# Kernel tuning notes

Hardware: AMD Instinct MI355X
Metric: run time of the kernel (lower is better)

The kernel has to match this reference:

```python
import jax, jax.numpy as jnp
import numpy as np


def setup_inputs() -> dict:
    key = jax.random.key(0)
    k1, k2, k3 = jax.random.split(key, 3)
    T, B, E = 2048, 2, 1024
    x = jax.random.normal(k1, (T, B, E), dtype=jnp.float32)
    # xavier-uniform-ish scaled weights
    in_weight = jax.random.normal(k2, (3 * E, E), dtype=jnp.float32) * (1.0 / np.sqrt(E))
    in_bias = jnp.zeros((3 * E,), dtype=jnp.float32)
    out_weight = jax.random.normal(k3, (E, E), dtype=jnp.float32) * (1.0 / np.sqrt(E))
    out_bias = jnp.zeros((E,), dtype=jnp.float32)
    return {"x": x, "in_weight": in_weight, "in_bias": in_bias,
            "out_weight": out_weight, "out_bias": out_bias, "n_heads": 16}


def reference(x, in_weight, in_bias, out_weight, out_bias, n_heads):
    # x: [T, B, E] time-major, self-attention (query is key is value)
    T, B, E = x.shape
    H = n_heads
    hd = E // H
    scale = hd ** -0.5
    # fused in-projection: [T, B, 3E]
    qkv = jnp.einsum('tbe,fe->tbf', x, in_weight) + in_bias
    q, k, v = jnp.split(qkv, 3, axis=-1)
    q = q * scale
    # [T, B, E] -> [B*H, T, hd]
    def to_heads(t):
        return t.reshape(T, B * H, hd).transpose(1, 0, 2)
    q, k, v = to_heads(q), to_heads(k), to_heads(v)
    # attention scores [B*H, T, T]
    attn_weights = jnp.einsum('nqd,nkd->nqk', q, k)
    attn_weights = jax.nn.softmax(attn_weights, axis=-1)
    # dropout p=0.0 (eval) -> identity
    attn = jnp.einsum('nqk,nkd->nqd', attn_weights, v)  # [B*H, T, hd]
    attn = attn.transpose(1, 0, 2).reshape(T, B, E)
    out = jnp.einsum('tbe,fe->tbf', attn, out_weight) + out_bias
    # need_weights=True: average over heads -> [B, T, T]
    avg_weights = attn_weights.reshape(B, H, T, T).sum(axis=1) / H
    return out, avg_weights
```

## Files before the change

kernel.cpp:

```cpp
#include <hip/hip_runtime.h>


#define T_DIM 2048
#define B_DIM 2
#define E_DIM 1024
#define H_DIM 16
#define HD 64
#define F_DIM 3072
#define M_DIM (T_DIM * B_DIM)
#define SCALE 0.125f

typedef __attribute__((ext_vector_type(8))) short bf16x8;
typedef __attribute__((ext_vector_type(4))) float f32x4;

__device__ inline unsigned short f2bf(float f) {
    union { float f; unsigned u; } v; v.f = f;
    unsigned r = v.u + 0x7fff + ((v.u >> 16) & 1);
    return (unsigned short)(r >> 16);
}

__global__ __launch_bounds__(256) void cast_bf16(
    const float* __restrict__ src, unsigned short* __restrict__ dst, int n8)
{
    int i = blockIdx.x * 256 + threadIdx.x;
    if (i >= n8) return;
    float4 a = *(const float4*)&src[i * 8];
    float4 b = *(const float4*)&src[i * 8 + 4];
    bf16x8 o;
    o[0] = f2bf(a.x); o[1] = f2bf(a.y); o[2] = f2bf(a.z); o[3] = f2bf(a.w);
    o[4] = f2bf(b.x); o[5] = f2bf(b.y); o[6] = f2bf(b.z); o[7] = f2bf(b.w);
    *(bf16x8*)&dst[i * 8] = o;
}

template <int MODE>
__global__ __launch_bounds__(256) void gemm_bf16(
    const unsigned short* __restrict__ A, const unsigned short* __restrict__ W,
    const float* __restrict__ bias,
    unsigned short* __restrict__ qb, unsigned short* __restrict__ kb,
    unsigned short* __restrict__ vb, float* __restrict__ outp)
{
    __shared__ short As[128][72];
    __shared__ short Bs[128][72];

    const int tid  = threadIdx.x;
    const int lane = tid & 63;
    const int wv   = tid >> 6;
    const int l16  = lane & 15;
    const int g    = lane >> 4;
    const int wr   = wv >> 1, wc = wv & 1;
    const int n0   = blockIdx.x * 128, m0 = blockIdx.y * 128;

    const int srow = tid >> 2;
    const int sc   = (tid & 3) * 16;

    f32x4 acc[4][4] = {};

    for (int k0 = 0; k0 < E_DIM; k0 += 64) {
        __syncthreads();
#pragma unroll
        for (int i = 0; i < 2; ++i) {
            const int row = srow + i * 64;
            const size_t ga = (size_t)(m0 + row) * E_DIM + k0 + sc;
            const size_t gb = (size_t)(n0 + row) * E_DIM + k0 + sc;
            *(bf16x8*)&As[row][sc]     = *(const bf16x8*)&A[ga];
            *(bf16x8*)&As[row][sc + 8] = *(const bf16x8*)&A[ga + 8];
            *(bf16x8*)&Bs[row][sc]     = *(const bf16x8*)&W[gb];
            *(bf16x8*)&Bs[row][sc + 8] = *(const bf16x8*)&W[gb + 8];
        }
        __syncthreads();

        bf16x8 af[4][2], bf[4][2];
#pragma unroll
        for (int mt = 0; mt < 4; ++mt) {
            af[mt][0] = *(const bf16x8*)&As[wr * 64 + mt * 16 + l16][g * 8];
            af[mt][1] = *(const bf16x8*)&As[wr * 64 + mt * 16 + l16][32 + g * 8];
        }
#pragma unroll
        for (int nt = 0; nt < 4; ++nt) {
            bf[nt][0] = *(const bf16x8*)&Bs[wc * 64 + nt * 16 + l16][g * 8];
            bf[nt][1] = *(const bf16x8*)&Bs[wc * 64 + nt * 16 + l16][32 + g * 8];
        }
#pragma unroll
        for (int mt = 0; mt < 4; ++mt)
#pragma unroll
            for (int nt = 0; nt < 4; ++nt) {
                acc[mt][nt] = __builtin_amdgcn_mfma_f32_16x16x32_bf16(
                    af[mt][0], bf[nt][0], acc[mt][nt], 0, 0, 0);
                acc[mt][nt] = __builtin_amdgcn_mfma_f32_16x16x32_bf16(
                    af[mt][1], bf[nt][1], acc[mt][nt], 0, 0, 0);
            }
    }

#pragma unroll
    for (int mt = 0; mt < 4; ++mt)
#pragma unroll
        for (int nt = 0; nt < 4; ++nt)
#pragma unroll
            for (int rr = 0; rr < 4; ++rr) {
                const int r = m0 + wr * 64 + mt * 16 + g * 4 + rr;
                const int f = n0 + wc * 64 + nt * 16 + l16;
                float val = acc[mt][nt][rr] + bias[f];
                if (MODE == 0) {
                    const int t = r >> 1, b = r & 1;
                    const int sec = f >> 10, rem = f & 1023;
                    const int h = rem >> 6, d = rem & 63;
                    const size_t idx = ((size_t)(b * H_DIM + h) * T_DIM + t) * HD + d;
                    if (sec == 0)      qb[idx] = f2bf(val * SCALE);
                    else if (sec == 1) kb[idx] = f2bf(val);
                    else               vb[idx] = f2bf(val);
                } else {
                    outp[(size_t)r * E_DIM + f] = val;
                }
            }
}

__global__ __launch_bounds__(256) void flash_kernel(
    const unsigned short* __restrict__ qb, const unsigned short* __restrict__ kb,
    const unsigned short* __restrict__ vb, unsigned short* __restrict__ ctxbuf,
    float2* __restrict__ ml)
{
    __shared__ short Ks[64][72];
    __shared__ short Vt[64][72];
    __shared__ short Ps[64][72];

    const int tid  = threadIdx.x;
    const int lane = tid & 63;
    const int w    = tid >> 6;
    const int l16  = lane & 15;
    const int g    = lane >> 4;
    const int q0   = blockIdx.x * 64;
    const int n    = blockIdx.y;
    const int b    = n >> 4, h = n & 15;

    const int krow = tid >> 2, kd0 = (tid & 3) << 4;
    const int vrow = tid & 63, vd0 = (tid >> 6) << 4;

    const size_t qrow = (size_t)n * T_DIM + q0 + w * 16 + l16;
    bf16x8 qf0 = *(const bf16x8*)&qb[qrow * HD + g * 8];
    bf16x8 qf1 = *(const bf16x8*)&qb[qrow * HD + 32 + g * 8];

    f32x4 ctx[4] = {};
    float m_[4], l_[4];
#pragma unroll
    for (int r = 0; r < 4; ++r) { m_[r] = -1e30f; l_[r] = 0.f; }

    for (int kt = 0; kt < T_DIM; kt += 64) {
        __syncthreads();
        const size_t kgrow = (size_t)n * T_DIM + kt;
        *(bf16x8*)&Ks[krow][kd0]     = *(const bf16x8*)&kb[(kgrow + krow) * HD + kd0];
        *(bf16x8*)&Ks[krow][kd0 + 8] = *(const bf16x8*)&kb[(kgrow + krow) * HD + kd0 + 8];
        bf16x8 v0 = *(const bf16x8*)&vb[(kgrow + vrow) * HD + vd0];
        bf16x8 v1 = *(const bf16x8*)&vb[(kgrow + vrow) * HD + vd0 + 8];
#pragma unroll
        for (int e = 0; e < 8; ++e) {
            Vt[vd0 + e][vrow]     = v0[e];
            Vt[vd0 + 8 + e][vrow] = v1[e];
        }
        __syncthreads();

        f32x4 s[4];
#pragma unroll
        for (int nt = 0; nt < 4; ++nt) {
            bf16x8 kf0 = *(const bf16x8*)&Ks[nt * 16 + l16][g * 8];
            bf16x8 kf1 = *(const bf16x8*)&Ks[nt * 16 + l16][32 + g * 8];
            f32x4 z = {0.f, 0.f, 0.f, 0.f};
            z = __builtin_amdgcn_mfma_f32_16x16x32_bf16(qf0, kf0, z, 0, 0, 0);
            z = __builtin_amdgcn_mfma_f32_16x16x32_bf16(qf1, kf1, z, 0, 0, 0);
            s[nt] = z;
        }

        float p[4][4];
#pragma unroll
        for (int r = 0; r < 4; ++r) {
            float mt = fmaxf(fmaxf(s[0][r], s[1][r]), fmaxf(s[2][r], s[3][r]));
            mt = fmaxf(mt, __shfl_xor(mt, 1));
            mt = fmaxf(mt, __shfl_xor(mt, 2));
            mt = fmaxf(mt, __shfl_xor(mt, 4));
            mt = fmaxf(mt, __shfl_xor(mt, 8));
            float mnew = fmaxf(m_[r], mt);
            float f = __expf(m_[r] - mnew);
            float rs = 0.f;
#pragma unroll
            for (int nt = 0; nt < 4; ++nt) { p[nt][r] = __expf(s[nt][r] - mnew); rs += p[nt][r]; }
            rs += __shfl_xor(rs, 1);
            rs += __shfl_xor(rs, 2);
            rs += __shfl_xor(rs, 4);
            rs += __shfl_xor(rs, 8);
            l_[r] = l_[r] * f + rs;
            m_[r] = mnew;
#pragma unroll
            for (int dt = 0; dt < 4; ++dt) ctx[dt][r] *= f;
        }

#pragma unroll
        for (int nt = 0; nt < 4; ++nt)
#pragma unroll
            for (int r = 0; r < 4; ++r)
                Ps[w * 16 + g * 4 + r][nt * 16 + l16] = (short)f2bf(p[nt][r]);

        bf16x8 pa0 = *(const bf16x8*)&Ps[w * 16 + l16][g * 8];
        bf16x8 pa1 = *(const bf16x8*)&Ps[w * 16 + l16][32 + g * 8];
#pragma unroll
        for (int dt = 0; dt < 4; ++dt) {
            bf16x8 vf0 = *(const bf16x8*)&Vt[dt * 16 + l16][g * 8];
            bf16x8 vf1 = *(const bf16x8*)&Vt[dt * 16 + l16][32 + g * 8];
            ctx[dt] = __builtin_amdgcn_mfma_f32_16x16x32_bf16(pa0, vf0, ctx[dt], 0, 0, 0);
            ctx[dt] = __builtin_amdgcn_mfma_f32_16x16x32_bf16(pa1, vf1, ctx[dt], 0, 0, 0);
        }
    }

    float linv[4];
#pragma unroll
    for (int r = 0; r < 4; ++r) linv[r] = 1.0f / l_[r];

#pragma unroll
    for (int dt = 0; dt < 4; ++dt)
#pragma unroll
        for (int r = 0; r < 4; ++r) {
            const int q = q0 + w * 16 + g * 4 + r;
            const int d = dt * 16 + l16;
            ctxbuf[((size_t)q * B_DIM + b) * E_DIM + h * HD + d] = f2bf(ctx[dt][r] * linv[r]);
        }

    if (l16 == 0) {
#pragma unroll
        for (int r = 0; r < 4; ++r)
            ml[(size_t)n * T_DIM + q0 + w * 16 + g * 4 + r] = make_float2(m_[r], linv[r]);
    }
}

__global__ __launch_bounds__(256) void avg_kernel(
    const unsigned short* __restrict__ qb, const unsigned short* __restrict__ kb,
    const float2* __restrict__ ml, float* __restrict__ avg)
{
    __shared__ short Kh[64][72];

    const int tid  = threadIdx.x;
    const int lane = tid & 63;
    const int w    = tid >> 6;
    const int l16  = lane & 15;
    const int g    = lane >> 4;
    const int kt0  = blockIdx.x * 64;
    const int q0   = blockIdx.y * 64;
    const int b    = blockIdx.z;

    const int krow = tid >> 2, kd0 = (tid & 3) << 4;

    f32x4 acc[4] = {};

    for (int h = 0; h < H_DIM; ++h) {
        const int n = b * H_DIM + h;
        __syncthreads();
        const size_t kgrow = (size_t)n * T_DIM + kt0;
        *(bf16x8*)&Kh[krow][kd0]     = *(const bf16x8*)&kb[(kgrow + krow) * HD + kd0];
        *(bf16x8*)&Kh[krow][kd0 + 8] = *(const bf16x8*)&kb[(kgrow + krow) * HD + kd0 + 8];
        __syncthreads();

        const size_t qrow = (size_t)n * T_DIM + q0 + w * 16 + l16;
        bf16x8 qf0 = *(const bf16x8*)&qb[qrow * HD + g * 8];
        bf16x8 qf1 = *(const bf16x8*)&qb[qrow * HD + 32 + g * 8];

        float2 mlv[4];
#pragma unroll
        for (int r = 0; r < 4; ++r)
            mlv[r] = ml[(size_t)n * T_DIM + q0 + w * 16 + g * 4 + r];

#pragma unroll
        for (int nt = 0; nt < 4; ++nt) {
            bf16x8 kf0 = *(const bf16x8*)&Kh[nt * 16 + l16][g * 8];
            bf16x8 kf1 = *(const bf16x8*)&Kh[nt * 16 + l16][32 + g * 8];
            f32x4 z = {0.f, 0.f, 0.f, 0.f};
            z = __builtin_amdgcn_mfma_f32_16x16x32_bf16(qf0, kf0, z, 0, 0, 0);
            z = __builtin_amdgcn_mfma_f32_16x16x32_bf16(qf1, kf1, z, 0, 0, 0);
#pragma unroll
            for (int r = 0; r < 4; ++r)
                acc[nt][r] += __expf(z[r] - mlv[r].x) * mlv[r].y * (1.0f / H_DIM);
        }
    }

#pragma unroll
    for (int nt = 0; nt < 4; ++nt)
#pragma unroll
        for (int r = 0; r < 4; ++r) {
            const int q = q0 + w * 16 + g * 4 + r;
            avg[((size_t)b * T_DIM + q) * T_DIM + kt0 + nt * 16 + l16] = acc[nt][r];
        }
}

extern "C" void kernel_launch(void* const* d_in, const int* in_sizes, int n_in,
                              void* d_out, int out_size, void* d_ws, size_t ws_size,
                              hipStream_t stream)
{
    const float* x     = (const float*)d_in[0];
    const float* w_in  = (const float*)d_in[1];
    const float* b_in  = (const float*)d_in[2];
    const float* w_out = (const float*)d_in[3];
    const float* b_out = (const float*)d_in[4];

    float* out = (float*)d_out;
    float* avg = out + (size_t)T_DIM * B_DIM * E_DIM;

    const size_t HSZ = (size_t)B_DIM * H_DIM * T_DIM * HD;
    unsigned short* qb   = (unsigned short*)d_ws;
    unsigned short* kb   = qb + HSZ;
    unsigned short* vb   = kb + HSZ;
    unsigned short* ctxb = vb + HSZ;
    unsigned short* xb   = ctxb + (size_t)T_DIM * B_DIM * E_DIM;
    unsigned short* wbin = xb + (size_t)T_DIM * B_DIM * E_DIM;
    unsigned short* wbot = wbin + (size_t)F_DIM * E_DIM;
    float2* ml = (float2*)(wbot + (size_t)E_DIM * E_DIM);

    cast_bf16<<<(T_DIM * B_DIM * E_DIM / 8 + 255) / 256, 256, 0, stream>>>(
        x, xb, T_DIM * B_DIM * E_DIM / 8);
    cast_bf16<<<(F_DIM * E_DIM / 8 + 255) / 256, 256, 0, stream>>>(
        w_in, wbin, F_DIM * E_DIM / 8);
    cast_bf16<<<(E_DIM * E_DIM / 8 + 255) / 256, 256, 0, stream>>>(
        w_out, wbot, E_DIM * E_DIM / 8);

    gemm_bf16<0><<<dim3(F_DIM / 128, M_DIM / 128), 256, 0, stream>>>(
        xb, wbin, b_in, qb, kb, vb, nullptr);

    flash_kernel<<<dim3(T_DIM / 64, B_DIM * H_DIM), 256, 0, stream>>>(
        qb, kb, vb, ctxb, ml);

    avg_kernel<<<dim3(T_DIM / 64, T_DIM / 64, B_DIM), 256, 0, stream>>>(
        qb, kb, ml, avg);

    gemm_bf16<1><<<dim3(E_DIM / 128, M_DIM / 128), 256, 0, stream>>>(
        ctxb, wbot, b_out, nullptr, nullptr, nullptr, out);
}
```

Measured before the change: 328.5 us.

## Prefetch K/V tiles into registers and widen avg kernel query tile

The flash kernel now loads the next K/V tile into registers while the current tile is written to shared memory and computed on, hiding global load latency. The avg kernel likewise prefetches the next head's K tile and processes 128 query rows per block instead of 64, halving the grid and reusing each staged K tile across two query sub-tiles. The bf16 conversion helper now calls the library __float2bfloat16 routine. The changes raise register pressure, which may reduce occupancy.

Result: slower. 338.0 us (+2.9%).

```diff
diff --git a/kernel.cpp b/kernel.cpp
--- a/kernel.cpp
+++ b/kernel.cpp
@@ -1,4 +1,5 @@
 #include <hip/hip_runtime.h>
+#include <hip/hip_bf16.h>
 
 
 #define T_DIM 2048
@@ -14,9 +15,9 @@
 typedef __attribute__((ext_vector_type(4))) float f32x4;
 
 __device__ inline unsigned short f2bf(float f) {
-    union { float f; unsigned u; } v; v.f = f;
-    unsigned r = v.u + 0x7fff + ((v.u >> 16) & 1);
-    return (unsigned short)(r >> 16);
+    union { __hip_bfloat16 h; unsigned short u; } v;
+    v.h = __float2bfloat16(f);
+    return v.u;
 }
 
 __global__ __launch_bounds__(256) void cast_bf16(
@@ -144,17 +145,27 @@
 #pragma unroll
     for (int r = 0; r < 4; ++r) { m_[r] = -1e30f; l_[r] = 0.f; }
 
+    const size_t hbase = (size_t)n * T_DIM;
+    bf16x8 kreg0 = *(const bf16x8*)&kb[(hbase + krow) * HD + kd0];
+    bf16x8 kreg1 = *(const bf16x8*)&kb[(hbase + krow) * HD + kd0 + 8];
+    bf16x8 vreg0 = *(const bf16x8*)&vb[(hbase + vrow) * HD + vd0];
+    bf16x8 vreg1 = *(const bf16x8*)&vb[(hbase + vrow) * HD + vd0 + 8];
+
     for (int kt = 0; kt < T_DIM; kt += 64) {
         __syncthreads();
-        const size_t kgrow = (size_t)n * T_DIM + kt;
-        *(bf16x8*)&Ks[krow][kd0]     = *(const bf16x8*)&kb[(kgrow + krow) * HD + kd0];
-        *(bf16x8*)&Ks[krow][kd0 + 8] = *(const bf16x8*)&kb[(kgrow + krow) * HD + kd0 + 8];
-        bf16x8 v0 = *(const bf16x8*)&vb[(kgrow + vrow) * HD + vd0];
-        bf16x8 v1 = *(const bf16x8*)&vb[(kgrow + vrow) * HD + vd0 + 8];
+        *(bf16x8*)&Ks[krow][kd0]     = kreg0;
+        *(bf16x8*)&Ks[krow][kd0 + 8] = kreg1;
 #pragma unroll
         for (int e = 0; e < 8; ++e) {
-            Vt[vd0 + e][vrow]     = v0[e];
-            Vt[vd0 + 8 + e][vrow] = v1[e];
+            Vt[vd0 + e][vrow]     = vreg0[e];
+            Vt[vd0 + 8 + e][vrow] = vreg1[e];
+        }
+        if (kt + 64 < T_DIM) {
+            const size_t kg = hbase + kt + 64;
+            kreg0 = *(const bf16x8*)&kb[(kg + krow) * HD + kd0];
+            kreg1 = *(const bf16x8*)&kb[(kg + krow) * HD + kd0 + 8];
+            vreg0 = *(const bf16x8*)&vb[(kg + vrow) * HD + vd0];
+            vreg1 = *(const bf16x8*)&vb[(kg + vrow) * HD + vd0 + 8];
         }
         __syncthreads();
 
@@ -241,50 +252,62 @@
     const int l16  = lane & 15;
     const int g    = lane >> 4;
     const int kt0  = blockIdx.x * 64;
-    const int q0   = blockIdx.y * 64;
+    const int q0   = blockIdx.y * 128;
     const int b    = blockIdx.z;
 
     const int krow = tid >> 2, kd0 = (tid & 3) << 4;
 
-    f32x4 acc[4] = {};
+    f32x4 acc[2][4] = {};
+
+    bf16x8 kreg0 = *(const bf16x8*)&kb[((size_t)(b * H_DIM) * T_DIM + kt0 + krow) * HD + kd0];
+    bf16x8 kreg1 = *(const bf16x8*)&kb[((size_t)(b * H_DIM) * T_DIM + kt0 + krow) * HD + kd0 + 8];
 
     for (int h = 0; h < H_DIM; ++h) {
         const int n = b * H_DIM + h;
         __syncthreads();
-        const size_t kgrow = (size_t)n * T_DIM + kt0;
-        *(bf16x8*)&Kh[krow][kd0]     = *(const bf16x8*)&kb[(kgrow + krow) * HD + kd0];
-        *(bf16x8*)&Kh[krow][kd0 + 8] = *(const bf16x8*)&kb[(kgrow + krow) * HD + kd0 + 8];
-        __syncthreads();
-
-        const size_t qrow = (size_t)n * T_DIM + q0 + w * 16 + l16;
-        bf16x8 qf0 = *(const bf16x8*)&qb[qrow * HD + g * 8];
-        bf16x8 qf1 = *(const bf16x8*)&qb[qrow * HD + 32 + g * 8];
-
-        float2 mlv[4];
-#pragma unroll
-        for (int r = 0; r < 4; ++r)
-            mlv[r] = ml[(size_t)n * T_DIM + q0 + w * 16 + g * 4 + r];
-
-#pragma unroll
-        for (int nt = 0; nt < 4; ++nt) {
-            bf16x8 kf0 = *(const bf16x8*)&Kh[nt * 16 + l16][g * 8];
-            bf16x8 kf1 = *(const bf16x8*)&Kh[nt * 16 + l16][32 + g * 8];
-            f32x4 z = {0.f, 0.f, 0.f, 0.f};
-            z = __builtin_amdgcn_mfma_f32_16x16x32_bf16(qf0, kf0, z, 0, 0, 0);
-            z = __builtin_amdgcn_mfma_f32_16x16x32_bf16(qf1, kf1, z, 0, 0, 0);
+        *(bf16x8*)&Kh[krow][kd0]     = kreg0;
+        *(bf16x8*)&Kh[krow][kd0 + 8] = kreg1;
+        if (h + 1 < H_DIM) {
+            const size_t kg = (size_t)(n + 1) * T_DIM + kt0 + krow;
+            kreg0 = *(const bf16x8*)&kb[kg * HD + kd0];
+            kreg1 = *(const bf16x8*)&kb[kg * HD + kd0 + 8];
+        }
+        __syncthreads();
+
+#pragma unroll
+        for (int qt = 0; qt < 2; ++qt) {
+            const size_t qrow = (size_t)n * T_DIM + q0 + qt * 64 + w * 16 + l16;
+            bf16x8 qf0 = *(const bf16x8*)&qb[qrow * HD + g * 8];
+            bf16x8 qf1 = *(const bf16x8*)&qb[qrow * HD + 32 + g * 8];
+
+            float2 mlv[4];
 #pragma unroll
             for (int r = 0; r < 4; ++r)
-                acc[nt][r] += __expf(z[r] - mlv[r].x) * mlv[r].y * (1.0f / H_DIM);
+                mlv[r] = ml[(size_t)n * T_DIM + q0 + qt * 64 + w * 16 + g * 4 + r];
+
+#pragma unroll
+            for (int nt = 0; nt < 4; ++nt) {
+                bf16x8 kf0 = *(const bf16x8*)&Kh[nt * 16 + l16][g * 8];
+                bf16x8 kf1 = *(const bf16x8*)&Kh[nt * 16 + l16][32 + g * 8];
+                f32x4 z = {0.f, 0.f, 0.f, 0.f};
+                z = __builtin_amdgcn_mfma_f32_16x16x32_bf16(qf0, kf0, z, 0, 0, 0);
+                z = __builtin_amdgcn_mfma_f32_16x16x32_bf16(qf1, kf1, z, 0, 0, 0);
+#pragma unroll
+                for (int r = 0; r < 4; ++r)
+                    acc[qt][nt][r] += __expf(z[r] - mlv[r].x) * mlv[r].y * (1.0f / H_DIM);
+            }
         }
     }
 
 #pragma unroll
-    for (int nt = 0; nt < 4; ++nt)
-#pragma unroll
-        for (int r = 0; r < 4; ++r) {
-            const int q = q0 + w * 16 + g * 4 + r;
-            avg[((size_t)b * T_DIM + q) * T_DIM + kt0 + nt * 16 + l16] = acc[nt][r];
-        }
+    for (int qt = 0; qt < 2; ++qt)
+#pragma unroll
+        for (int nt = 0; nt < 4; ++nt)
+#pragma unroll
+            for (int r = 0; r < 4; ++r) {
+                const int q = q0 + qt * 64 + w * 16 + g * 4 + r;
+                avg[((size_t)b * T_DIM + q) * T_DIM + kt0 + nt * 16 + l16] = acc[qt][nt][r];
+            }
 }
 
 extern "C" void kernel_launch(void* const* d_in, const int* in_sizes, int n_in,
@@ -323,7 +346,7 @@
     flash_kernel<<<dim3(T_DIM / 64, B_DIM * H_DIM), 256, 0, stream>>>(
         qb, kb, vb, ctxb, ml);
 
-    avg_kernel<<<dim3(T_DIM / 64, T_DIM / 64, B_DIM), 256, 0, stream>>>(
+    avg_kernel<<<dim3(T_DIM / 64, T_DIM / 128, B_DIM), 256, 0, stream>>>(
         qb, kb, ml, avg);
 
     gemm_bf16<1><<<dim3(E_DIM / 128, M_DIM / 128), 256, 0, stream>>>(
```
